# Kernel tuning notes

Hardware: AMD Instinct MI355X
Metric: run time of the kernel (lower is better)

The kernel has to match this reference:

```python
import jax, jax.numpy as jnp
import numpy as np


def setup_inputs() -> dict:
    key = jax.random.key(0)
    k1, k2 = jax.random.split(key)
    B, S, H = 16, 512, 512
    x = jax.random.normal(k1, (B, S, H), dtype=jnp.float32)
    durations = jax.random.randint(k2, (B, S), 0, 16, dtype=jnp.int32)
    return {"x": x, "durations": durations, "max_len": 4096}


def reference(x, durations, max_len):
    # x: [B, S, H] float, durations: [B, S] int, max_len: python int
    B, S, H = x.shape
    # Inclusive cumulative end positions of each token's expanded span.
    cum = jnp.cumsum(durations, axis=1)                      # [B, S]
    t = jnp.arange(max_len, dtype=cum.dtype)                 # [T]
    # For output frame t, source token j is the first with cum[j] > t.
    idx = jax.vmap(lambda c: jnp.searchsorted(c, t, side='right'))(cum)  # [B, T]
    valid = idx < S                                          # frames beyond total stay zero
    idx_c = jnp.minimum(idx, S - 1)
    out = jnp.take_along_axis(x, idx_c[:, :, None], axis=1)  # [B, T, H]
    return jnp.where(valid[:, :, None], out, jnp.zeros((), dtype=x.dtype))
```

## Files before the change

kernel.cpp:

```cpp
#include <hip/hip_runtime.h>
#include <hip/hip_bf16.h>

#define SCAN_BLOCK 512

typedef __attribute__((ext_vector_type(4))) float f32x4;

__global__ __launch_bounds__(SCAN_BLOCK)
void lr_buildmap_kernel(const int* __restrict__ dur, int* __restrict__ map,
                        const int* __restrict__ T_ptr, int BS, int BT) {
    const int T = *T_ptr;
    const int B = BT / T;
    const int S = BS / B;
    __shared__ int sdata[SCAN_BLOCK];
    const int tid = threadIdx.x;
    for (int row = blockIdx.x; row < B; row += gridDim.x) {
        int carry = 0;
        for (int base = 0; base < S; base += SCAN_BLOCK) {
            const int n = min(SCAN_BLOCK, S - base);
            __syncthreads();
            const int v = (tid < n) ? dur[row * S + base + tid] : 0;
            sdata[tid] = v;
            __syncthreads();
            #pragma unroll
            for (int off = 1; off < SCAN_BLOCK; off <<= 1) {
                int add = (tid >= off) ? sdata[tid - off] : 0;
                __syncthreads();
                sdata[tid] += add;
                __syncthreads();
            }
            if (tid < n) {
                const int inc   = sdata[tid] + carry;
                const int end   = min(inc, T);
                const int start = min(inc - v, T);
                const int tok   = row * S + base + tid;
                for (int t = start; t < end; ++t) map[row * T + t] = tok;
            }
            carry += sdata[SCAN_BLOCK - 1];
        }
        __syncthreads();
        const int total = min(carry, T);
        for (int t = total + tid; t < T; t += SCAN_BLOCK) map[row * T + t] = -1;
    }
}

__global__ __launch_bounds__(256)
void lr_expand_kernel(const f32x4* __restrict__ x, const int* __restrict__ map,
                      f32x4* __restrict__ out, int n4, int shift) {
    const int g = blockIdx.x * blockDim.x + threadIdx.x;
    if (g >= n4) return;
    const int frame = g >> shift;
    const int lane  = g & ((1 << shift) - 1);
    const int tok   = map[frame];
    f32x4 v = (f32x4)(0.f, 0.f, 0.f, 0.f);
    if (tok >= 0) v = x[((size_t)tok << shift) + lane];
    __builtin_nontemporal_store(v, &out[g]);
}

extern "C" void kernel_launch(void* const* d_in, const int* in_sizes, int n_in,
                              void* d_out, int out_size, void* d_ws, size_t ws_size,
                              hipStream_t stream) {
    const float* x     = (const float*)d_in[0];
    const int*   dur   = (const int*)d_in[1];
    const int*   T_ptr = (const int*)d_in[2];

    const int BSH = in_sizes[0];
    const int BS  = in_sizes[1];
    const int H   = BSH / BS;
    const int BT  = out_size / H;
    const int H4  = H / 4;
    const int shift = __builtin_ctz(H4);

    int* map = (int*)d_ws;

    lr_buildmap_kernel<<<64, SCAN_BLOCK, 0, stream>>>(dur, map, T_ptr, BS, BT);

    const int n4 = out_size / 4;
    const int grid = (n4 + 255) / 256;
    lr_expand_kernel<<<grid, 256, 0, stream>>>((const f32x4*)x, map, (f32x4*)d_out,
                                               n4, shift);
}
```

Baseline: 169.5 us.

## Fuse duration scan and frame gather into one kernel with binary search

```diff
diff --git a/kernel.cpp b/kernel.cpp
--- a/kernel.cpp
+++ b/kernel.cpp
@@ -1,59 +1,84 @@
 #include <hip/hip_runtime.h>
-#include <hip/hip_bf16.h>
 
-#define SCAN_BLOCK 512
+#define THREADS 256
+#define FPB 32
+#define MAX_S 2048
 
 typedef __attribute__((ext_vector_type(4))) float f32x4;
 
-__global__ __launch_bounds__(SCAN_BLOCK)
-void lr_buildmap_kernel(const int* __restrict__ dur, int* __restrict__ map,
-                        const int* __restrict__ T_ptr, int BS, int BT) {
-    const int T = *T_ptr;
-    const int B = BT / T;
-    const int S = BS / B;
-    __shared__ int sdata[SCAN_BLOCK];
-    const int tid = threadIdx.x;
-    for (int row = blockIdx.x; row < B; row += gridDim.x) {
-        int carry = 0;
-        for (int base = 0; base < S; base += SCAN_BLOCK) {
-            const int n = min(SCAN_BLOCK, S - base);
-            __syncthreads();
-            const int v = (tid < n) ? dur[row * S + base + tid] : 0;
-            sdata[tid] = v;
-            __syncthreads();
-            #pragma unroll
-            for (int off = 1; off < SCAN_BLOCK; off <<= 1) {
-                int add = (tid >= off) ? sdata[tid - off] : 0;
-                __syncthreads();
-                sdata[tid] += add;
-                __syncthreads();
+__global__ __launch_bounds__(THREADS)
+void lr_fused_kernel(const f32x4* __restrict__ x, const int* __restrict__ dur,
+                     const int* __restrict__ T_ptr, f32x4* __restrict__ out,
+                     int BS, int BT, int shift ) {
+    const int T  = *T_ptr;
+    const int B  = BT / T;
+    const int S  = BS / B;
+    const int H4 = 1 << shift;
+
+    __shared__ int cum[MAX_S];
+    __shared__ int wsum[THREADS / 64];
+    __shared__ int tokidx[FPB];
+
+    const int nwg = gridDim.x;
+    int l = blockIdx.x;
+    if ((nwg & 7) == 0) {
+        const int cpx = nwg >> 3;
+        l = (l & 7) * cpx + (l >> 3);
+    }
+
+    const int frame0 = l * FPB;
+    if (frame0 >= BT) return;
+    const int row     = frame0 / T;
+    const int rframe0 = frame0 - row * T;
+    const int tid     = threadIdx.x;
+
+    int carry = 0;
+    for (int base = 0; base < S; base += THREADS) {
+        const int idx = base + tid;
+        int v = (idx < S) ? dur[row * S + idx] : 0;
+        #pragma unroll
+        for (int off = 1; off < 64; off <<= 1) {
+            int t = __shfl_up(v, off, 64);
+            if ((tid & 63) >= off) v += t;
+        }
+        if ((tid & 63) == 63) wsum[tid >> 6] = v;
+        __syncthreads();
+        int woff = carry;
+        #pragma unroll
+        for (int w = 0; w < THREADS / 64; ++w)
+            if (w < (tid >> 6)) woff += wsum[w];
+        if (idx < S) cum[idx] = v + woff;
+        carry += wsum[0] + wsum[1] + wsum[2] + wsum[3];
+        __syncthreads();
+    }
+
+    if (tid < FPB) {
+        const int f = rframe0 + tid;
+        const int total = cum[S - 1];
+        int tok = -1;
+        if (f < T && f < total) {
+            int lo = 0, hi = S;
+            while (lo < hi) {
+                const int mid = (lo + hi) >> 1;
+                if (cum[mid] > f) hi = mid; else lo = mid + 1;
             }
-            if (tid < n) {
-                const int inc   = sdata[tid] + carry;
-                const int end   = min(inc, T);
-                const int start = min(inc - v, T);
-                const int tok   = row * S + base + tid;
-                for (int t = start; t < end; ++t) map[row * T + t] = tok;
-            }
-            carry += sdata[SCAN_BLOCK - 1];
+            tok = row * S + lo;
         }
-        __syncthreads();
-        const int total = min(carry, T);
-        for (int t = total + tid; t < T; t += SCAN_BLOCK) map[row * T + t] = -1;
+        tokidx[tid] = tok;
     }
-}
+    __syncthreads();
 
-__global__ __launch_bounds__(256)
-void lr_expand_kernel(const f32x4* __restrict__ x, const int* __restrict__ map,
-                      f32x4* __restrict__ out, int n4, int shift) {
-    const int g = blockIdx.x * blockDim.x + threadIdx.x;
-    if (g >= n4) return;
-    const int frame = g >> shift;
-    const int lane  = g & ((1 << shift) - 1);
-    const int tok   = map[frame];
-    f32x4 v = (f32x4)(0.f, 0.f, 0.f, 0.f);
-    if (tok >= 0) v = x[((size_t)tok << shift) + lane];
-    __builtin_nontemporal_store(v, &out[g]);
+    const size_t outbase = (size_t)frame0 << shift;
+    const int    total4  = FPB << shift;
+    const int    nthis   = min(total4, (int)(((size_t)BT << shift) - outbase));
+    for (int i = tid; i < nthis; i += THREADS) {
+        const int f    = i >> shift;
+        const int lane = i & (H4 - 1);
+        const int tok  = tokidx[f];
+        f32x4 v = (f32x4)(0.f, 0.f, 0.f, 0.f);
+        if (tok >= 0) v = x[((size_t)tok << shift) + lane];
+        __builtin_nontemporal_store(v, &out[outbase + i]);
+    }
 }
 
 extern "C" void kernel_launch(void* const* d_in, const int* in_sizes, int n_in,
@@ -70,12 +95,7 @@
     const int H4  = H / 4;
     const int shift = __builtin_ctz(H4);
 
-    int* map = (int*)d_ws;
-
-    lr_buildmap_kernel<<<64, SCAN_BLOCK, 0, stream>>>(dur, map, T_ptr, BS, BT);
-
-    const int n4 = out_size / 4;
-    const int grid = (n4 + 255) / 256;
-    lr_expand_kernel<<<grid, 256, 0, stream>>>((const f32x4*)x, map, (f32x4*)d_out,
-                                               n4, shift);
+    const int grid = (BT + FPB - 1) / FPB;
+    lr_fused_kernel<<<grid, THREADS, 0, stream>>>((const f32x4*)x, dur, T_ptr,
+                                                  (f32x4*)d_out, BS, BT, shift);
 }
```

After: 164.6 us. -2.9%, faster.
